# Kernel optimization log

Hardware: AMD Instinct MI355X
Metric: run time of the kernel (lower is better)

## Reference

```python
import jax, jax.numpy as jnp
import numpy as np

N, E, G = 100000, 1600000, 256   # nodes, edges, graphs
D, H, OUT, STEPS = 128, 128, 2, 4
EPS = 1e-5


def _bn(x, g, b):
    # BatchNorm1d training-mode math: biased batch stats
    mu = jnp.mean(x, axis=0)
    var = jnp.var(x, axis=0)
    return g * (x - mu) * jax.lax.rsqrt(var + EPS) + b


def setup_inputs() -> dict:
    key = jax.random.key(0)
    ks = jax.random.split(key, 20)
    s = 0.05
    return {
        "x": jax.random.normal(ks[0], (N, D), dtype=jnp.float32),
        "edge_index": jax.random.randint(ks[1], (2, E), 0, N, dtype=jnp.int32),
        "batch": jnp.sort(jax.random.randint(ks[2], (N,), 0, G, dtype=jnp.int32)),
        "W_in": jax.random.normal(ks[3], (H, D), dtype=jnp.float32) * s,
        "b_in": jnp.zeros((H,), jnp.float32),
        "bn1_g": jnp.ones((H,), jnp.float32),
        "bn1_b": jnp.zeros((H,), jnp.float32),
        "ggc_w": jax.random.normal(ks[4], (STEPS, H, H), dtype=jnp.float32) * s,
        "gru_wih": jax.random.normal(ks[5], (3 * H, H), dtype=jnp.float32) * s,
        "gru_whh": jax.random.normal(ks[6], (3 * H, H), dtype=jnp.float32) * s,
        "gru_bih": jnp.zeros((3 * H,), jnp.float32),
        "gru_bhh": jnp.zeros((3 * H,), jnp.float32),
        "bn2_g": jnp.ones((H,), jnp.float32),
        "bn2_b": jnp.zeros((H,), jnp.float32),
        "W1": jax.random.normal(ks[7], (H, 2 * H), dtype=jnp.float32) * s,
        "b1": jnp.zeros((H,), jnp.float32),
        "bn3_g": jnp.ones((H,), jnp.float32),
        "bn3_b": jnp.zeros((H,), jnp.float32),
        "W2": jax.random.normal(ks[8], (OUT, H), dtype=jnp.float32) * s,
        "b2": jnp.zeros((OUT,), jnp.float32),
    }


def reference(x, edge_index, batch, W_in, b_in, bn1_g, bn1_b, ggc_w,
              gru_wih, gru_whh, gru_bih, gru_bhh, bn2_g, bn2_b,
              W1, b1, bn3_g, bn3_b, W2, b2):
    src, dst = edge_index[0], edge_index[1]

    h = x @ W_in.T + b_in
    h = jax.nn.relu(_bn(h, bn1_g, bn1_b))
    skip = h

    # GatedGraphConv: per-step linear -> scatter-add aggregation -> GRUCell
    for i in range(STEPS):
        m = h @ ggc_w[i]                                   # [N,H]
        agg = jax.ops.segment_sum(m[src], dst, num_segments=N)  # [N,H]
        gi = agg @ gru_wih.T + gru_bih                     # [N,3H]
        gh = h @ gru_whh.T + gru_bhh                       # [N,3H]
        i_r, i_z, i_n = jnp.split(gi, 3, axis=1)
        h_r, h_z, h_n = jnp.split(gh, 3, axis=1)
        r = jax.nn.sigmoid(i_r + h_r)
        z = jax.nn.sigmoid(i_z + h_z)
        n = jnp.tanh(i_n + r * h_n)
        h = (1.0 - z) * n + z * h

    h = jax.nn.relu(_bn(h, bn2_g, bn2_b) + skip)

    # global_mean_pool (source uses it for both "mean" and "max" branches)
    cnt = jnp.maximum(jax.ops.segment_sum(jnp.ones((N,), h.dtype), batch, num_segments=G), 1.0)
    mean = jax.ops.segment_sum(h, batch, num_segments=G) / cnt[:, None]  # [G,H]
    pooled = jnp.concatenate([mean, mean], axis=1)                        # [G,2H]

    y = jax.nn.relu(_bn(pooled @ W1.T + b1, bn3_g, bn3_b))
    return y @ W2.T + b2
```

## Files before the change

kernel.cpp:

```cpp
#include <hip/hip_runtime.h>
#include <math.h>


#define EPSV 1e-5f

typedef __attribute__((ext_vector_type(8))) short bf16x8;
typedef __attribute__((ext_vector_type(4))) float f32x4;

__device__ __forceinline__ float fsig(float x){
  return 1.0f/(1.0f+__expf(-x));
}
__device__ __forceinline__ float ftanh(float x){
  float ax = fabsf(x);
  float e = __expf(-2.0f*ax);
  float r = (1.0f-e)/(1.0f+e);
  return copysignf(r, x);
}
__device__ __forceinline__ unsigned short bf16rne(float x){
  unsigned u = __float_as_uint(x);
  unsigned r = (u + 0x7FFFu + ((u>>16)&1u)) >> 16;
  return (unsigned short)r;
}
__device__ __forceinline__ float bf16tof(unsigned short h){
  return __uint_as_float(((unsigned)h)<<16);
}

__global__ void k_zero(float* __restrict__ p, int n){
  int i = blockIdx.x*256+threadIdx.x;
  if (i<n) p[i]=0.0f;
}

__global__ void k_prep(const float* __restrict__ Win, float* __restrict__ Wq,
                       const float* __restrict__ W1, float* __restrict__ W1cT){
  int i = blockIdx.x*256+threadIdx.x;
  if (i < 16384){
    int k=i>>7, j=i&127;
    Wq[(k>>2)*512 + j*4 + (k&3)] = Win[j*128+k];
  } else if (i < 32768){
    int r=i-16384; int j=r>>7, o=r&127;
    W1cT[j*128+o] = W1[o*256+j] + W1[o*256+128+j];
  }
}

__global__ void k_prepB(const float* __restrict__ ggc, const float* __restrict__ wih,
                        const float* __restrict__ whh,
                        short* __restrict__ Bhi, short* __restrict__ Blo){
  int i = blockIdx.x*256+threadIdx.x;
  int st = i>>17;
  int r  = i&131071;
  int k  = r>>9;
  int c  = r&511;
  int gr = c>>7, j = c&127;
  float val = 0.f;
  if (k<128){
    if (gr<3){
      const float* g = ggc + st*16384 + k*128;
      const float* w = wih + (gr*128+j)*128;
      float acc=0.f;
      for (int m=0;m<128;m++) acc += g[m]*w[m];
      val = acc;
    }
  } else {
    int kh = k-128;
    if (gr!=2){
      int gate = (gr==3)?2:gr;
      val = whh[(gate*128+j)*128 + kh];
    }
  }
  unsigned short h = bf16rne(val);
  unsigned short lo = bf16rne(val - bf16tof(h));
  size_t off = (size_t)st*131072 + ((size_t)(k>>5)*512 + (size_t)c)*32 + (size_t)(k&31);
  Bhi[off]=(short)h; Blo[off]=(short)lo;
}

__global__ __launch_bounds__(256,2) void k_gemm_in(
    const float* __restrict__ x, const float* __restrict__ Wq, const float* __restrict__ bin,
    float* __restrict__ X, float* __restrict__ sumP, float* __restrict__ sqP, int N)
{
  __shared__ __align__(16) float xl[32][128];
  __shared__ float red[2][128];
  int t=threadIdx.x;
  int nbase = blockIdx.x*32;
  for (int it=0; it<4; ++it){
    int f4 = it*256+t;
    int n = f4>>5; int k=(f4&31)*4;
    int gn=nbase+n;
    float4 v = make_float4(0.f,0.f,0.f,0.f);
    if (gn<N) v = *(const float4*)&x[(size_t)gn*128+k];
    *(float4*)&xl[n][k]=v;
  }
  __syncthreads();
  int j=t&127, half=t>>7, nb=half*16;
  float acc[16];
  #pragma unroll
  for (int q=0;q<16;q++) acc[q]=0.f;
  for (int k=0;k<128;k+=4){
    float4 w = *(const float4*)&Wq[(k>>2)*512 + j*4];
    #pragma unroll
    for (int q=0;q<16;q++){
      float4 xv = *(const float4*)&xl[nb+q][k];
      acc[q] += xv.x*w.x + xv.y*w.y + xv.z*w.z + xv.w*w.w;
    }
  }
  float bv = bin[j];
  float ts=0.f, tq=0.f;
  #pragma unroll
  for (int q=0;q<16;q++){
    int n=nbase+nb+q;
    if (n<N){
      float tv=acc[q]+bv;
      X[(size_t)n*128+j]=tv;
      ts+=tv; tq+=tv*tv;
    }
  }
  int p = (blockIdx.x&63)*128+j;
  red[half][j]=ts; __syncthreads();
  if (half==0) atomicAdd(&sumP[p], red[0][j]+red[1][j]);
  __syncthreads();
  red[half][j]=tq; __syncthreads();
  if (half==0) atomicAdd(&sqP[p], red[0][j]+red[1][j]);
}

__global__ void k_bn_fin(const float* __restrict__ sumP, const float* __restrict__ sqP, int P, float invcnt,
                         const float* __restrict__ g, const float* __restrict__ b,
                         float* __restrict__ sc, float* __restrict__ sh){
  int j = threadIdx.x;
  if (j>=128) return;
  float s=0.f,q=0.f;
  for (int p=0;p<P;p++){ s+=sumP[p*128+j]; q+=sqP[p*128+j]; }
  float mu = s*invcnt;
  float var = fmaxf(q*invcnt - mu*mu, 0.f);
  float scale = g[j]*rsqrtf(var+EPSV);
  sc[j]=scale; sh[j]=b[j]-mu*scale;
}

__global__ void k_apply_bn1(const float4* __restrict__ X, const float* __restrict__ sc,
                            const float* __restrict__ sh, float4* __restrict__ h0, int total4){
  int i = blockIdx.x*256+threadIdx.x;
  if (i>=total4) return;
  float4 t = X[i];
  int j0 = (i*4)&127;
  float4 s = *(const float4*)&sc[j0];
  float4 b = *(const float4*)&sh[j0];
  float4 o;
  o.x = fmaxf(t.x*s.x+b.x, 0.f);
  o.y = fmaxf(t.y*s.y+b.y, 0.f);
  o.z = fmaxf(t.z*s.z+b.z, 0.f);
  o.w = fmaxf(t.w*s.w+b.w, 0.f);
  h0[i]=o;
}

__global__ void k_hist(const int* __restrict__ dst, int* __restrict__ deg, int E){
  int e = blockIdx.x*256+threadIdx.x;
  if (e<E) atomicAdd(&deg[dst[e]], 1);
}
__global__ void k_scan1(const int* __restrict__ deg, int* __restrict__ rowptr, int* __restrict__ bsum, int N){
  __shared__ int tmp[256];
  int t=threadIdx.x; int n=blockIdx.x*256+t;
  int v = (n<N)?deg[n]:0;
  tmp[t]=v;
  __syncthreads();
  for (int o=1;o<256;o<<=1){
    int add = (t>=o)? tmp[t-o] : 0;
    __syncthreads();
    tmp[t]+=add;
    __syncthreads();
  }
  if (n<N) rowptr[n+1]=tmp[t];
  if (t==255) bsum[blockIdx.x]=tmp[255];
}
__global__ void k_scan2(int* bsum, int nb, int* rowptr){
  __shared__ int tmp[512];
  int t=threadIdx.x;
  int v = (t<nb)? bsum[t] : 0;
  tmp[t]=v; __syncthreads();
  for (int o=1;o<512;o<<=1){
    int add = (t>=o)? tmp[t-o] : 0;
    __syncthreads();
    tmp[t]+=add;
    __syncthreads();
  }
  if (t<nb) bsum[t]=tmp[t]-v;
  if (t==0) rowptr[0]=0;
}
__global__ void k_scan3(int* rowptr, const int* __restrict__ bsum, int N){
  int n = blockIdx.x*256+threadIdx.x;
  if (n<N) rowptr[n+1] += bsum[blockIdx.x];
}
__global__ void k_fill(const int* __restrict__ ei, int* __restrict__ deg,
                       const int* __restrict__ rowptr, int* __restrict__ col, int E){
  int e = blockIdx.x*256+threadIdx.x;
  if (e<E){
    int d = ei[E+e];
    int old = atomicSub(&deg[d],1);
    col[rowptr[d] + old - 1] = ei[e];
  }
}

__global__ __launch_bounds__(256,8) void k_agg(
    const float* __restrict__ h, float* __restrict__ s,
    const int* __restrict__ rowptr, const int* __restrict__ col, int N)
{
  int wave = (blockIdx.x*256+threadIdx.x)>>6;
  int lane = threadIdx.x&63;
  if (wave>=N) return;
  int e = rowptr[wave], e1 = rowptr[wave+1];
  float2 a0=make_float2(0.f,0.f), a1=a0, a2=a0, a3=a0;
  for (; e+3<e1; e+=4){
    int c0=col[e],c1=col[e+1],c2=col[e+2],c3=col[e+3];
    float2 v0 = *(const float2*)&h[(size_t)c0*128+lane*2];
    float2 v1 = *(const float2*)&h[(size_t)c1*128+lane*2];
    float2 v2 = *(const float2*)&h[(size_t)c2*128+lane*2];
    float2 v3 = *(const float2*)&h[(size_t)c3*128+lane*2];
    a0.x+=v0.x; a0.y+=v0.y; a1.x+=v1.x; a1.y+=v1.y;
    a2.x+=v2.x; a2.y+=v2.y; a3.x+=v3.x; a3.y+=v3.y;
  }
  for (; e<e1; e++){
    int c0=col[e];
    float2 v0 = *(const float2*)&h[(size_t)c0*128+lane*2];
    a0.x+=v0.x; a0.y+=v0.y;
  }
  float2 r;
  r.x=(a0.x+a1.x)+(a2.x+a3.x);
  r.y=(a0.y+a1.y)+(a2.y+a3.y);
  *(float2*)&s[(size_t)wave*128+lane*2]=r;
}

__global__ __launch_bounds__(256,2) void k_gru_mfma(
    const float* __restrict__ s, const float* __restrict__ hin, float* __restrict__ hout,
    const short* __restrict__ Bhi, const short* __restrict__ Blo,
    const float* __restrict__ bih, const float* __restrict__ bhh, int N,
    float* __restrict__ sumP, float* __restrict__ sqP)
{
  __shared__ __align__(16) short Abuf[2*32*256];
  short* Ahi = Abuf;
  short* Alo = Abuf + 32*256;
  int t = threadIdx.x;
  int nbase = blockIdx.x*32;

  for (int it=0; it<8; ++it){
    int f4 = it*256 + t;
    int row = f4>>6;
    int c4  = f4&63;
    int k   = c4*4;
    int n   = nbase + row;
    float4 v = make_float4(0.f,0.f,0.f,0.f);
    if (n < N){
      const float* src = (k<128) ? &s[(size_t)n*128 + k] : &hin[(size_t)n*128 + (k-128)];
      v = *(const float4*)src;
    }
    unsigned short h0=bf16rne(v.x), h1=bf16rne(v.y), h2=bf16rne(v.z), h3=bf16rne(v.w);
    unsigned short l0=bf16rne(v.x-bf16tof(h0)), l1=bf16rne(v.y-bf16tof(h1));
    unsigned short l2=bf16rne(v.z-bf16tof(h2)), l3=bf16rne(v.w-bf16tof(h3));
    int g = c4>>1, half = c4&1;
    int gs = g ^ (row&7);
    int off = row*256 + gs*8 + half*4;
    uint2 H; H.x = (unsigned)h0 | ((unsigned)h1<<16); H.y = (unsigned)h2 | ((unsigned)h3<<16);
    uint2 L; L.x = (unsigned)l0 | ((unsigned)l1<<16); L.y = (unsigned)l2 | ((unsigned)l3<<16);
    *(uint2*)&Ahi[off] = H;
    *(uint2*)&Alo[off] = L;
  }
  __syncthreads();

  int wv = t>>6, l = t&63;
  int lj = l&15, lk = l>>4;

  f32x4 acc[2][8];
  #pragma unroll
  for (int mt=0; mt<2; ++mt)
    #pragma unroll
    for (int nt=0; nt<8; ++nt)
      acc[mt][nt] = (f32x4){0.f,0.f,0.f,0.f};

#define DO_GR(GR_) { \
    _Pragma("unroll") \
    for (int jt=0; jt<2; ++jt){ \
      int c  = (GR_)*128 + wv*32 + jt*16 + lj; \
      size_t boff = ((size_t)kc*512 + (size_t)c)*32 + (size_t)lk*8; \
      bf16x8 b_hi = *(const bf16x8*)&Bhi[boff]; \
      bf16x8 b_lo = *(const bf16x8*)&Blo[boff]; \
      acc[0][(GR_)*2+jt] = __builtin_amdgcn_mfma_f32_16x16x32_bf16(a_hi[0], b_hi, acc[0][(GR_)*2+jt], 0,0,0); \
      acc[1][(GR_)*2+jt] = __builtin_amdgcn_mfma_f32_16x16x32_bf16(a_hi[1], b_hi, acc[1][(GR_)*2+jt], 0,0,0); \
      acc[0][(GR_)*2+jt] = __builtin_amdgcn_mfma_f32_16x16x32_bf16(a_lo[0], b_hi, acc[0][(GR_)*2+jt], 0,0,0); \
      acc[1][(GR_)*2+jt] = __builtin_amdgcn_mfma_f32_16x16x32_bf16(a_lo[1], b_hi, acc[1][(GR_)*2+jt], 0,0,0); \
      acc[0][(GR_)*2+jt] = __builtin_amdgcn_mfma_f32_16x16x32_bf16(a_hi[0], b_lo, acc[0][(GR_)*2+jt], 0,0,0); \
      acc[1][(GR_)*2+jt] = __builtin_amdgcn_mfma_f32_16x16x32_bf16(a_hi[1], b_lo, acc[1][(GR_)*2+jt], 0,0,0); \
    } }

  for (int kc=0; kc<4; ++kc){
    bf16x8 a_hi[2], a_lo[2];
    #pragma unroll
    for (int mt=0; mt<2; ++mt){
      int r = mt*16 + lj;
      int g = kc*4 + lk;
      int off = r*256 + ((g ^ (r&7))<<3);
      a_hi[mt] = *(bf16x8*)&Ahi[off];
      a_lo[mt] = *(bf16x8*)&Alo[off];
    }
    DO_GR(0) DO_GR(1) DO_GR(2)
  }
  for (int kc=4; kc<8; ++kc){
    bf16x8 a_hi[2], a_lo[2];
    #pragma unroll
    for (int mt=0; mt<2; ++mt){
      int r = mt*16 + lj;
      int g = kc*4 + lk;
      int off = r*256 + ((g ^ (r&7))<<3);
      a_hi[mt] = *(bf16x8*)&Ahi[off];
      a_lo[mt] = *(bf16x8*)&Alo[off];
    }
    DO_GR(0) DO_GR(1) DO_GR(3)
  }
#undef DO_GR

  float holdv[2][2][4];
  #pragma unroll
  for (int jt=0; jt<2; ++jt){
    int j = wv*32 + jt*16 + lj;
    int g = 16 + (j>>3);
    int pos = j&7;
    #pragma unroll
    for (int mt=0; mt<2; ++mt){
      #pragma unroll
      for (int rg=0; rg<4; ++rg){
        int row = mt*16 + lk*4 + rg;
        int off = row*256 + ((g ^ (row&7))<<3) + pos;
        holdv[jt][mt][rg] = bf16tof((unsigned short)Ahi[off]) + bf16tof((unsigned short)Alo[off]);
      }
    }
  }

  float hvv[2][2][4];
  #pragma unroll
  for (int jt=0; jt<2; ++jt){
    int j = wv*32 + jt*16 + lj;
    float br=bih[j], bz=bih[128+j], bn_=bih[256+j];
    float cr=bhh[j], cz=bhh[128+j], cn=bhh[256+j];
    float ts=0.f, tq=0.f;
    #pragma unroll
    for (int mt=0; mt<2; ++mt){
      #pragma unroll
      for (int rg=0; rg<4; ++rg){
        float r  = fsig(acc[mt][0+jt][rg] + br + cr);
        float z  = fsig(acc[mt][2+jt][rg] + bz + cz);
        float nn = ftanh(acc[mt][4+jt][rg] + bn_ + r*(acc[mt][6+jt][rg] + cn));
        float hv = (1.f-z)*nn + z*holdv[jt][mt][rg];
        hvv[jt][mt][rg] = hv;
        ts += hv; tq += hv*hv;
      }
    }
    if (sumP){
      atomicAdd(&sumP[(blockIdx.x&63)*128 + j], ts);
      atomicAdd(&sqP [(blockIdx.x&63)*128 + j], tq);
    }
  }

  __syncthreads();
  float* O = (float*)Abuf;
  #pragma unroll
  for (int jt=0; jt<2; ++jt){
    int j = wv*32 + jt*16 + lj;
    #pragma unroll
    for (int mt=0; mt<2; ++mt){
      #pragma unroll
      for (int rg=0; rg<4; ++rg){
        int row = mt*16 + lk*4 + rg;
        O[row*132 + j] = hvv[jt][mt][rg];
      }
    }
  }
  __syncthreads();
  for (int it=0; it<4; ++it){
    int idx = it*256 + t;
    int row = idx>>5, c4 = idx&31;
    int n = nbase + row;
    if (n < N){
      *(float4*)&hout[(size_t)n*128 + c4*4] = *(float4*)&O[row*132 + c4*4];
    }
  }
}

__global__ void k_bn2_pool(const float* __restrict__ hfin, const float* __restrict__ h0,
                           const int* __restrict__ batch, const float* __restrict__ sc,
                           const float* __restrict__ sh, float* __restrict__ pool,
                           float* __restrict__ cntf, int N){
  int t=threadIdx.x, j=t&127, half=t>>7;
  int n0 = blockIdx.x*256 + half*128;
  float scv=sc[j], shv=sh[j];
  int curg=-1; float acc=0.f, cacc=0.f;
  for (int r=0;r<128;r++){
    int n=n0+r; if (n>=N) break;
    int g = batch[n];
    float v = fmaxf(hfin[(size_t)n*128+j]*scv+shv + h0[(size_t)n*128+j], 0.f);
    if (g!=curg){
      if (curg>=0){
        atomicAdd(&pool[curg*128+j], acc);
        if (j==0) atomicAdd(&cntf[curg], cacc);
      }
      curg=g; acc=0.f; cacc=0.f;
    }
    acc+=v; cacc+=1.f;
  }
  if (curg>=0){
    atomicAdd(&pool[curg*128+j], acc);
    if (j==0) atomicAdd(&cntf[curg], cacc);
  }
}

__global__ void k_head1(const float* __restrict__ pool, const float* __restrict__ cntf,
                        const float* __restrict__ W1cT, const float* __restrict__ b1,
                        float* __restrict__ t3, float* __restrict__ sum3, float* __restrict__ sq3){
  __shared__ float mean[128];
  int g=blockIdx.x, o=threadIdx.x;
  float inv = 1.0f/fmaxf(cntf[g],1.0f);
  mean[o] = pool[g*128+o]*inv;
  __syncthreads();
  float acc=0.f;
  for (int jj=0;jj<128;jj++) acc += mean[jj]*W1cT[jj*128+o];
  float v = acc + b1[o];
  t3[g*128+o]=v;
  atomicAdd(&sum3[o], v);
  atomicAdd(&sq3[o], v*v);
}

__global__ void k_head2(const float* __restrict__ t3, const float* __restrict__ sc,
                        const float* __restrict__ sh, const float* __restrict__ W2,
                        const float* __restrict__ b2, float* __restrict__ out){
  __shared__ float y[128];
  int g=blockIdx.x, o=threadIdx.x;
  float v = fmaxf(t3[g*128+o]*sc[o]+sh[o], 0.f);
  y[o]=v; __syncthreads();
  if (o<2){
    float acc=b2[o];
    for (int k=0;k<128;k++) acc += y[k]*W2[o*128+k];
    out[g*2+o]=acc;
  }
}

extern "C" void kernel_launch(void* const* d_in, const int* in_sizes, int n_in,
                              void* d_out, int out_size, void* d_ws, size_t ws_size,
                              hipStream_t stream){
  (void)n_in; (void)ws_size;
  const float* x    = (const float*)d_in[0];
  const int*   ei   = (const int*)d_in[1];
  const int*   batch= (const int*)d_in[2];
  const float* W_in = (const float*)d_in[3];
  const float* b_in = (const float*)d_in[4];
  const float* bn1_g= (const float*)d_in[5];
  const float* bn1_b= (const float*)d_in[6];
  const float* ggc  = (const float*)d_in[7];
  const float* wih  = (const float*)d_in[8];
  const float* whh  = (const float*)d_in[9];
  const float* bih  = (const float*)d_in[10];
  const float* bhh  = (const float*)d_in[11];
  const float* bn2_g= (const float*)d_in[12];
  const float* bn2_b= (const float*)d_in[13];
  const float* W1   = (const float*)d_in[14];
  const float* b1   = (const float*)d_in[15];
  const float* bn3_g= (const float*)d_in[16];
  const float* bn3_b= (const float*)d_in[17];
  const float* W2   = (const float*)d_in[18];
  const float* b2   = (const float*)d_in[19];
  float* out = (float*)d_out;

  int N = in_sizes[0]/128;
  int E = in_sizes[1]/2;
  int G = out_size/2;

  char* ws = (char*)d_ws;
  size_t off=0;
  auto alloc=[&](size_t bytes)->char*{
    char* p = ws+off; off = (off+bytes+255) & ~(size_t)255; return p;
  };
  float* buf0 = (float*)alloc((size_t)N*128*4);
  float* h0   = (float*)alloc((size_t)N*128*4);
  float* buf2 = (float*)alloc((size_t)N*128*4);
  short* Bhi  = (short*)alloc((size_t)4*131072*2);
  short* Blo  = (short*)alloc((size_t)4*131072*2);
  float* Wq   = (float*)alloc((size_t)16384*4);
  float* W1cT = (float*)alloc((size_t)16384*4);
  int* rowptr = (int*)alloc((size_t)(N+1)*4);
  int* col    = (int*)alloc((size_t)E*4);
  int* bsum   = (int*)alloc((size_t)512*4);
  float* t3   = (float*)alloc((size_t)G*128*4);
  float* sc1 = (float*)alloc(512); float* sh1 = (float*)alloc(512);
  float* sc2 = (float*)alloc(512); float* sh2 = (float*)alloc(512);
  float* sc3 = (float*)alloc(512); float* sh3 = (float*)alloc(512);
  char* zstart = ws+off;
  int*   deg  = (int*)alloc((size_t)N*4);
  float* sumP1= (float*)alloc((size_t)64*128*4);
  float* sqP1 = (float*)alloc((size_t)64*128*4);
  float* sumP2= (float*)alloc((size_t)64*128*4);
  float* sqP2 = (float*)alloc((size_t)64*128*4);
  float* sum3 = (float*)alloc(512);
  float* sq3  = (float*)alloc(512);
  float* pool = (float*)alloc((size_t)G*128*4);
  float* cntf = (float*)alloc((size_t)G*4);
  char* zend = ws+off;
  int zwords = (int)((zend - zstart)/4);

  int nbScan  = (N+255)/256;
  int gridN32 = (N+31)/32;
  int gridAgg = (N*64+255)/256;

  k_zero<<<(zwords+255)/256,256,0,stream>>>((float*)zstart, zwords);
  k_prep<<<128,256,0,stream>>>(W_in, Wq, W1, W1cT);
  k_prepB<<<2048,256,0,stream>>>(ggc, wih, whh, Bhi, Blo);

  k_hist<<<(E+255)/256,256,0,stream>>>(ei+E, deg, E);
  k_scan1<<<nbScan,256,0,stream>>>(deg, rowptr, bsum, N);
  k_scan2<<<1,512,0,stream>>>(bsum, nbScan, rowptr);
  k_scan3<<<nbScan,256,0,stream>>>(rowptr, bsum, N);
  k_fill<<<(E+255)/256,256,0,stream>>>(ei, deg, rowptr, col, E);

  k_gemm_in<<<gridN32,256,0,stream>>>(x, Wq, b_in, buf0, sumP1, sqP1, N);
  k_bn_fin<<<1,128,0,stream>>>(sumP1, sqP1, 64, 1.0f/(float)N, bn1_g, bn1_b, sc1, sh1);
  k_apply_bn1<<<(N*128/4+255)/256,256,0,stream>>>((const float4*)buf0, sc1, sh1, (float4*)h0, N*128/4);

  k_agg<<<gridAgg,256,0,stream>>>(h0,   buf0, rowptr, col, N);
  k_gru_mfma<<<gridN32,256,0,stream>>>(buf0, h0,   buf0, Bhi+0*131072, Blo+0*131072, bih, bhh, N, nullptr, nullptr);
  k_agg<<<gridAgg,256,0,stream>>>(buf0, buf2, rowptr, col, N);
  k_gru_mfma<<<gridN32,256,0,stream>>>(buf2, buf0, buf2, Bhi+1*131072, Blo+1*131072, bih, bhh, N, nullptr, nullptr);
  k_agg<<<gridAgg,256,0,stream>>>(buf2, buf0, rowptr, col, N);
  k_gru_mfma<<<gridN32,256,0,stream>>>(buf0, buf2, buf0, Bhi+2*131072, Blo+2*131072, bih, bhh, N, nullptr, nullptr);
  k_agg<<<gridAgg,256,0,stream>>>(buf0, buf2, rowptr, col, N);
  k_gru_mfma<<<gridN32,256,0,stream>>>(buf2, buf0, buf2, Bhi+3*131072, Blo+3*131072, bih, bhh, N, sumP2, sqP2);

  k_bn_fin<<<1,128,0,stream>>>(sumP2, sqP2, 64, 1.0f/(float)N, bn2_g, bn2_b, sc2, sh2);
  k_bn2_pool<<<(N+255)/256,256,0,stream>>>(buf2, h0, batch, sc2, sh2, pool, cntf, N);
  k_head1<<<G,128,0,stream>>>(pool, cntf, W1cT, b1, t3, sum3, sq3);
  k_bn_fin<<<1,128,0,stream>>>(sum3, sq3, 1, 1.0f/(float)G, bn3_g, bn3_b, sc3, sh3);
  k_head2<<<G,128,0,stream>>>(t3, sc3, sh3, W2, b2, out);
}
```

Measured before the change: 1.449 ms.

## Use 512-thread blocks in GRU MFMA kernel with one column tile per wave

The GRU MFMA kernel now launches 512 threads (8 waves) per 32-row block instead of 256, and each wave owns 16 output columns rather than 32. This halves the per-wave accumulator count and the number of B-fragment loads per wave, lowering register pressure and spreading the gate math over more waves. Staging and write-back loops are reindexed to match. The cost is more waves per block competing for the same LDS tile, and the total B traffic per block is unchanged.

```diff
diff --git a/kernel.cpp b/kernel.cpp
--- a/kernel.cpp
+++ b/kernel.cpp
@@ -226,7 +226,7 @@
   *(float2*)&s[(size_t)wave*128+lane*2]=r;
 }
 
-__global__ __launch_bounds__(256,2) void k_gru_mfma(
+__global__ __launch_bounds__(512,2) void k_gru_mfma(
     const float* __restrict__ s, const float* __restrict__ hin, float* __restrict__ hout,
     const short* __restrict__ Bhi, const short* __restrict__ Blo,
     const float* __restrict__ bih, const float* __restrict__ bhh, int N,
@@ -238,8 +238,8 @@
   int t = threadIdx.x;
   int nbase = blockIdx.x*32;
 
-  for (int it=0; it<8; ++it){
-    int f4 = it*256 + t;
+  for (int it=0; it<4; ++it){
+    int f4 = it*512 + t;
     int row = f4>>6;
     int c4  = f4&63;
     int k   = c4*4;
@@ -265,27 +265,25 @@
   int wv = t>>6, l = t&63;
   int lj = l&15, lk = l>>4;
 
-  f32x4 acc[2][8];
+  f32x4 acc[2][4];
   #pragma unroll
   for (int mt=0; mt<2; ++mt)
     #pragma unroll
-    for (int nt=0; nt<8; ++nt)
-      acc[mt][nt] = (f32x4){0.f,0.f,0.f,0.f};
-
-#define DO_GR(GR_) { \
-    _Pragma("unroll") \
-    for (int jt=0; jt<2; ++jt){ \
-      int c  = (GR_)*128 + wv*32 + jt*16 + lj; \
-      size_t boff = ((size_t)kc*512 + (size_t)c)*32 + (size_t)lk*8; \
-      bf16x8 b_hi = *(const bf16x8*)&Bhi[boff]; \
-      bf16x8 b_lo = *(const bf16x8*)&Blo[boff]; \
-      acc[0][(GR_)*2+jt] = __builtin_amdgcn_mfma_f32_16x16x32_bf16(a_hi[0], b_hi, acc[0][(GR_)*2+jt], 0,0,0); \
-      acc[1][(GR_)*2+jt] = __builtin_amdgcn_mfma_f32_16x16x32_bf16(a_hi[1], b_hi, acc[1][(GR_)*2+jt], 0,0,0); \
-      acc[0][(GR_)*2+jt] = __builtin_amdgcn_mfma_f32_16x16x32_bf16(a_lo[0], b_hi, acc[0][(GR_)*2+jt], 0,0,0); \
-      acc[1][(GR_)*2+jt] = __builtin_amdgcn_mfma_f32_16x16x32_bf16(a_lo[1], b_hi, acc[1][(GR_)*2+jt], 0,0,0); \
-      acc[0][(GR_)*2+jt] = __builtin_amdgcn_mfma_f32_16x16x32_bf16(a_hi[0], b_lo, acc[0][(GR_)*2+jt], 0,0,0); \
-      acc[1][(GR_)*2+jt] = __builtin_amdgcn_mfma_f32_16x16x32_bf16(a_hi[1], b_lo, acc[1][(GR_)*2+jt], 0,0,0); \
-    } }
+    for (int gt=0; gt<4; ++gt)
+      acc[mt][gt] = (f32x4){0.f,0.f,0.f,0.f};
+
+#define DO_G(G_) { \
+    int c  = (G_)*128 + wv*16 + lj; \
+    size_t boff = ((size_t)kc*512 + (size_t)c)*32 + (size_t)lk*8; \
+    bf16x8 b_hi = *(const bf16x8*)&Bhi[boff]; \
+    bf16x8 b_lo = *(const bf16x8*)&Blo[boff]; \
+    acc[0][G_] = __builtin_amdgcn_mfma_f32_16x16x32_bf16(a_hi[0], b_hi, acc[0][G_], 0,0,0); \
+    acc[1][G_] = __builtin_amdgcn_mfma_f32_16x16x32_bf16(a_hi[1], b_hi, acc[1][G_], 0,0,0); \
+    acc[0][G_] = __builtin_amdgcn_mfma_f32_16x16x32_bf16(a_lo[0], b_hi, acc[0][G_], 0,0,0); \
+    acc[1][G_] = __builtin_amdgcn_mfma_f32_16x16x32_bf16(a_lo[1], b_hi, acc[1][G_], 0,0,0); \
+    acc[0][G_] = __builtin_amdgcn_mfma_f32_16x16x32_bf16(a_hi[0], b_lo, acc[0][G_], 0,0,0); \
+    acc[1][G_] = __builtin_amdgcn_mfma_f32_16x16x32_bf16(a_hi[1], b_lo, acc[1][G_], 0,0,0); \
+  }
 
   for (int kc=0; kc<4; ++kc){
     bf16x8 a_hi[2], a_lo[2];
@@ -297,7 +295,7 @@
       a_hi[mt] = *(bf16x8*)&Ahi[off];
       a_lo[mt] = *(bf16x8*)&Alo[off];
     }
-    DO_GR(0) DO_GR(1) DO_GR(2)
+    DO_G(0) DO_G(1) DO_G(2)
   }
   for (int kc=4; kc<8; ++kc){
     bf16x8 a_hi[2], a_lo[2];
@@ -309,14 +307,13 @@
       a_hi[mt] = *(bf16x8*)&Ahi[off];
       a_lo[mt] = *(bf16x8*)&Alo[off];
     }
-    DO_GR(0) DO_GR(1) DO_GR(3)
-  }
-#undef DO_GR
-
-  float holdv[2][2][4];
-  #pragma unroll
-  for (int jt=0; jt<2; ++jt){
-    int j = wv*32 + jt*16 + lj;
+    DO_G(0) DO_G(1) DO_G(3)
+  }
+#undef DO_G
+
+  int j = wv*16 + lj;
+  float holdv[2][4];
+  {
     int g = 16 + (j>>3);
     int pos = j&7;
     #pragma unroll
@@ -325,15 +322,13 @@
       for (int rg=0; rg<4; ++rg){
         int row = mt*16 + lk*4 + rg;
         int off = row*256 + ((g ^ (row&7))<<3) + pos;
-        holdv[jt][mt][rg] = bf16tof((unsigned short)Ahi[off]) + bf16tof((unsigned short)Alo[off]);
+        holdv[mt][rg] = bf16tof((unsigned short)Ahi[off]) + bf16tof((unsigned short)Alo[off]);
       }
     }
   }
 
-  float hvv[2][2][4];
-  #pragma unroll
-  for (int jt=0; jt<2; ++jt){
-    int j = wv*32 + jt*16 + lj;
+  float hvv[2][4];
+  {
     float br=bih[j], bz=bih[128+j], bn_=bih[256+j];
     float cr=bhh[j], cz=bhh[128+j], cn=bhh[256+j];
     float ts=0.f, tq=0.f;
@@ -341,11 +336,11 @@
     for (int mt=0; mt<2; ++mt){
       #pragma unroll
       for (int rg=0; rg<4; ++rg){
-        float r  = fsig(acc[mt][0+jt][rg] + br + cr);
-        float z  = fsig(acc[mt][2+jt][rg] + bz + cz);
-        float nn = ftanh(acc[mt][4+jt][rg] + bn_ + r*(acc[mt][6+jt][rg] + cn));
-        float hv = (1.f-z)*nn + z*holdv[jt][mt][rg];
-        hvv[jt][mt][rg] = hv;
+        float r  = fsig(acc[mt][0][rg] + br + cr);
+        float z  = fsig(acc[mt][1][rg] + bz + cz);
+        float nn = ftanh(acc[mt][2][rg] + bn_ + r*(acc[mt][3][rg] + cn));
+        float hv = (1.f-z)*nn + z*holdv[mt][rg];
+        hvv[mt][rg] = hv;
         ts += hv; tq += hv*hv;
       }
     }
@@ -358,20 +353,16 @@
   __syncthreads();
   float* O = (float*)Abuf;
   #pragma unroll
-  for (int jt=0; jt<2; ++jt){
-    int j = wv*32 + jt*16 + lj;
-    #pragma unroll
-    for (int mt=0; mt<2; ++mt){
-      #pragma unroll
-      for (int rg=0; rg<4; ++rg){
-        int row = mt*16 + lk*4 + rg;
-        O[row*132 + j] = hvv[jt][mt][rg];
-      }
-    }
-  }
-  __syncthreads();
-  for (int it=0; it<4; ++it){
-    int idx = it*256 + t;
+  for (int mt=0; mt<2; ++mt){
+    #pragma unroll
+    for (int rg=0; rg<4; ++rg){
+      int row = mt*16 + lk*4 + rg;
+      O[row*132 + j] = hvv[mt][rg];
+    }
+  }
+  __syncthreads();
+  for (int it=0; it<2; ++it){
+    int idx = it*512 + t;
     int row = idx>>5, c4 = idx&31;
     int n = nbase + row;
     if (n < N){
@@ -518,13 +509,13 @@
   k_apply_bn1<<<(N*128/4+255)/256,256,0,stream>>>((const float4*)buf0, sc1, sh1, (float4*)h0, N*128/4);
 
   k_agg<<<gridAgg,256,0,stream>>>(h0,   buf0, rowptr, col, N);
-  k_gru_mfma<<<gridN32,256,0,stream>>>(buf0, h0,   buf0, Bhi+0*131072, Blo+0*131072, bih, bhh, N, nullptr, nullptr);
+  k_gru_mfma<<<gridN32,512,0,stream>>>(buf0, h0,   buf0, Bhi+0*131072, Blo+0*131072, bih, bhh, N, nullptr, nullptr);
   k_agg<<<gridAgg,256,0,stream>>>(buf0, buf2, rowptr, col, N);
-  k_gru_mfma<<<gridN32,256,0,stream>>>(buf2, buf0, buf2, Bhi+1*131072, Blo+1*131072, bih, bhh, N, nullptr, nullptr);
+  k_gru_mfma<<<gridN32,512,0,stream>>>(buf2, buf0, buf2, Bhi+1*131072, Blo+1*131072, bih, bhh, N, nullptr, nullptr);
   k_agg<<<gridAgg,256,0,stream>>>(buf2, buf0, rowptr, col, N);
-  k_gru_mfma<<<gridN32,256,0,stream>>>(buf0, buf2, buf0, Bhi+2*131072, Blo+2*131072, bih, bhh, N, nullptr, nullptr);
+  k_gru_mfma<<<gridN32,512,0,stream>>>(buf0, buf2, buf0, Bhi+2*131072, Blo+2*131072, bih, bhh, N, nullptr, nullptr);
   k_agg<<<gridAgg,256,0,stream>>>(buf0, buf2, rowptr, col, N);
-  k_gru_mfma<<<gridN32,256,0,stream>>>(buf2, buf0, buf2, Bhi+3*131072, Blo+3*131072, bih, bhh, N, sumP2, sqP2);
+  k_gru_mfma<<<gridN32,512,0,stream>>>(buf2, buf0, buf2, Bhi+3*131072, Blo+3*131072, bih, bhh, N, sumP2, sqP2);
 
   k_bn_fin<<<1,128,0,stream>>>(sumP2, sqP2, 64, 1.0f/(float)N, bn2_g, bn2_b, sc2, sh2);
   k_bn2_pool<<<(N+255)/256,256,0,stream>>>(buf2, h0, batch, sc2, sh2, pool, cntf, N);
```

Result: faster. 1.378 ms (-4.9%).
